# Kernel tuning notes

Hardware: AMD Instinct MI355X
Metric: run time of the kernel (lower is better)

The kernel has to match this reference:

```python
import jax, jax.numpy as jnp
import numpy as np

D, ED, N, R, K, NL = 128, 256, 16, 8, 4, 3   # d_model, d_inner, d_state, dt_rank, d_conv, n_layers
B, L = 4, 1024
HID, OUT = 256, 2
EPS = 1e-5


def setup_inputs() -> dict:
    key = jax.random.key(0)
    ks = jax.random.split(key, 16)
    g = lambda k, shape, s=0.05: jax.random.normal(k, shape, dtype=jnp.float32) * s
    return {
        "x": jax.random.normal(ks[0], (B, L, D), dtype=jnp.float32),
        # Mamba params, stacked over (2 directions, NL layers)
        "rms_w": jnp.ones((2, NL, D), jnp.float32),
        "in_w": g(ks[1], (2, NL, 2 * ED, D)),
        "in_b": g(ks[2], (2, NL, 2 * ED)),
        "conv_w": g(ks[3], (2, NL, ED, K)),
        "conv_b": g(ks[4], (2, NL, ED)),
        "xproj_w": g(ks[5], (2, NL, R + 2 * N, ED)),
        "dt_w": g(ks[6], (2, NL, ED, R)),
        "dt_b": g(ks[7], (2, NL, ED)),
        "A_log": jnp.broadcast_to(jnp.log(jnp.arange(1.0, N + 1.0, dtype=jnp.float32)), (2, NL, ED, N)) + 0.0,
        "Dp": jnp.ones((2, NL, ED), jnp.float32),
        "out_w": g(ks[8], (2, NL, D, ED)),
        "out_b": g(ks[9], (2, NL, D)),
        # MLP head params (BatchNorm in training mode: batch stats)
        "bn1_g": jnp.ones((2 * D,), jnp.float32), "bn1_b": jnp.zeros((2 * D,), jnp.float32),
        "w1": g(ks[10], (HID, 2 * D)), "b1": g(ks[11], (HID,)),
        "bn2_g": jnp.ones((HID,), jnp.float32), "bn2_b": jnp.zeros((HID,), jnp.float32),
        "w2": g(ks[12], (HID, HID)), "b2": g(ks[13], (HID,)),
        "bn3_g": jnp.ones((HID,), jnp.float32), "bn3_b": jnp.zeros((HID,), jnp.float32),
        "w3": g(ks[14], (OUT, HID)), "b3": g(ks[15], (OUT,)),
    }


def _rms(x, w):
    return x * jax.lax.rsqrt(jnp.mean(x * x, axis=-1, keepdims=True) + EPS) * w


def _dwconv(x, w, b):
    # causal depthwise conv; x: (B,L,ED), w: (ED,K)
    y = jax.lax.conv_general_dilated(x.transpose(0, 2, 1), w[:, None, :], (1,), [(K - 1, 0)],
                                     feature_group_count=ED, dimension_numbers=("NCH", "OIH", "NCH"))
    return y.transpose(0, 2, 1) + b


def _ssm(dA, dBx, C):
    # dA,dBx: (B,L,ED,N); C: (B,L,N) -> y: (B,L,ED)
    def step(h, inp):
        a, bx, c = inp
        h = a * h + bx
        return h, jnp.einsum("ben,bn->be", h, c)
    h0 = jnp.zeros((dA.shape[0], ED, N), dA.dtype)
    _, ys = jax.lax.scan(step, h0, (dA.transpose(1, 0, 2, 3), dBx.transpose(1, 0, 2, 3), C.transpose(1, 0, 2)))
    return ys.transpose(1, 0, 2)


def _block(x, in_w, in_b, conv_w, conv_b, xproj_w, dt_w, dt_b, A_log, Dp, out_w, out_b):
    xz = x @ in_w.T + in_b
    xi, z = xz[..., :ED], xz[..., ED:]
    xi = jax.nn.silu(_dwconv(xi, conv_w, conv_b))
    dbc = xi @ xproj_w.T
    dt, Bm, Cm = dbc[..., :R], dbc[..., R:R + N], dbc[..., R + N:]
    delta = jax.nn.softplus(dt @ dt_w.T + dt_b)            # (B,L,ED)
    A = -jnp.exp(A_log)                                    # (ED,N)
    dA = jnp.exp(delta[..., None] * A)                     # (B,L,ED,N)
    dBx = (delta * xi)[..., None] * Bm[:, :, None, :]      # (B,L,ED,N)
    y = _ssm(dA, dBx, Cm) + Dp * xi
    y = y * jax.nn.silu(z)
    return y @ out_w.T + out_b


def _mamba(x, d, rms_w, in_w, in_b, conv_w, conv_b, xproj_w, dt_w, dt_b, A_log, Dp, out_w, out_b):
    for l in range(NL):
        x = x + _block(_rms(x, rms_w[d, l]), in_w[d, l], in_b[d, l], conv_w[d, l], conv_b[d, l],
                       xproj_w[d, l], dt_w[d, l], dt_b[d, l], A_log[d, l], Dp[d, l], out_w[d, l], out_b[d, l])
    return x


def _bn(x, g, b):
    m = jnp.mean(x, axis=0)
    v = jnp.mean((x - m) ** 2, axis=0)  # biased var, torch BN training mode
    return (x - m) * jax.lax.rsqrt(v + EPS) * g + b


def _forward(x, rms_w, in_w, in_b, conv_w, conv_b, xproj_w, dt_w, dt_b, A_log, Dp, out_w, out_b,
             bn1_g, bn1_b, w1, b1, bn2_g, bn2_b, w2, b2, bn3_g, bn3_b, w3, b3):
    mp = (rms_w, in_w, in_b, conv_w, conv_b, xproj_w, dt_w, dt_b, A_log, Dp, out_w, out_b)
    fwd = _mamba(x, 0, *mp)
    bwd = jnp.flip(_mamba(jnp.flip(x, axis=1), 1, *mp), axis=1)
    h = jnp.concatenate([fwd, bwd], axis=2).reshape(B * L, 2 * D)
    h = jax.nn.leaky_relu(_bn(h, bn1_g, bn1_b) @ w1.T + b1)
    h = jax.nn.leaky_relu(_bn(h, bn2_g, bn2_b) @ w2.T + b2)
    h = _bn(h, bn3_g, bn3_b) @ w3.T + b3
    return h.reshape(B, L, OUT)


def reference(x, rms_w, in_w, in_b, conv_w, conv_b, xproj_w, dt_w, dt_b, A_log, Dp, out_w, out_b,
              bn1_g, bn1_b, w1, b1, bn2_g, bn2_b, w2, b2, bn3_g, bn3_b, w3, b3):
    return _forward(x, rms_w, in_w, in_b, conv_w, conv_b, xproj_w, dt_w, dt_b, A_log, Dp, out_w, out_b,
                    bn1_g, bn1_b, w1, b1, bn2_g, bn2_b, w2, b2, bn3_g, bn3_b, w3, b3)
```

## Files before the change

kernel.cpp:

```cpp
#include <hip/hip_runtime.h>
#include <hip/hip_bf16.h>
#include <hip/hip_fp16.h>

#define NL 3
#define EPS 1e-5f

#define C_INB    393984L
#define C_CONVW  397056L
#define C_CONVB  403200L
#define C_XPROJW 404736L
#define C_DTW    466176L
#define C_DTB    478464L
#define C_ALOG   480000L
#define C_DP     504576L
#define C_OUTB   702720L
#define C_BN1G   703488L
#define C_BN1B   703744L
#define C_B1     769536L
#define C_BN2G   769792L
#define C_BN2B   770048L
#define C_B2     835840L
#define C_BN3G   836096L
#define C_BN3B   836352L
#define C_W3     836608L
#define C_B3     837120L
#define FLAG_OFF 837184L
#define X0_OFF   837248L
#define X1_OFF   1361536L
#define XZT_OFF  1885824L
#define DBCT_OFF 8177280L
#define YGP_OFF  8504960L
#define BNA_OFF  10603648L
#define HINW_OFF  10605184L
#define HOUTW_OFF 10801792L
#define HW1_OFF   10900096L
#define HW2_OFF   10932864L
#define HXW_OFF   10965632L
#define H1_OFF   XZT_OFF
#define H2_OFF   (XZT_OFF + 1048576L)

#define ASLD 68

struct Ptrs { const void* p[25]; };

typedef _Float16 half8 __attribute__((ext_vector_type(8)));
typedef float f32x4 __attribute__((ext_vector_type(4)));

static __device__ const int  CV_SRC[21] = {0,0,3,4,5,6,7,8,9,10,12,13,14,16,17,18,20,21,22,23,24};
static __device__ const long CV_DST[21] = {X0_OFF,X1_OFF,C_INB,C_CONVW,C_CONVB,C_XPROJW,C_DTW,C_DTB,C_ALOG,C_DP,
                                           C_OUTB,C_BN1G,C_BN1B,C_B1,C_BN2G,C_BN2B,C_B2,C_BN3G,C_BN3B,C_W3,C_B3};
static __device__ const int  CV_SZ[21]  = {524288,524288,3072,6144,1536,61440,12288,1536,24576,1536,
                                           768,256,256,256,256,256,256,256,256,512,2};

__device__ inline float ldsrc(const void* s, long i, bool isbf) {
  if (isbf) { unsigned int u = ((const unsigned short*)s)[i]; return __uint_as_float(u << 16); }
  return ((const float*)s)[i];
}

__global__ __launch_bounds__(256) void g_convert(Ptrs ps, float* __restrict__ ws) {
  bool isbf = (*(const unsigned int*)ps.p[1]) == 0x3F803F80u;
  int job = blockIdx.y;
  if (job == 0 && blockIdx.x == 0 && threadIdx.x == 0) ws[FLAG_OFF] = isbf ? 1.f : 0.f;
  int tid0 = blockIdx.x * 256 + threadIdx.x;
  int stride = gridDim.x * 256;
  if (job < 21) {
    int n = CV_SZ[job];
    const void* s = ps.p[CV_SRC[job]];
    float* dp = ws + CV_DST[job];
    bool permute = (job < 2);
    for (int i = tid0; i < n; i += stride) {
      long si = i;
      if (permute) {
        int row = i >> 7, col = i & 127;
        int b = row >> 10, p = row & 1023;
        int t = ((p & 63) << 4) + (p >> 6);
        si = ((long)((b << 10) + t) << 7) + col;
      }
      dp[i] = ldsrc(s, si, isbf);
    }
  } else if (job == 21) {
    _Float16* dp = (_Float16*)(ws + HINW_OFF);
    const void* sw = ps.p[2]; const void* sr = ps.p[1];
    for (int i = tid0; i < 393216; i += stride) {
      int dl = i >> 16, k = i & 127;
      float v = ldsrc(sw, i, isbf) * ldsrc(sr, dl*128 + k, isbf);
      dp[i] = (_Float16)v;
    }
  } else if (job == 22) {
    _Float16* dp = (_Float16*)(ws + HOUTW_OFF);
    const void* s = ps.p[11];
    for (int i = tid0; i < 196608; i += stride) dp[i] = (_Float16)ldsrc(s, i, isbf);
  } else if (job == 23) {
    _Float16* dp = (_Float16*)(ws + HW1_OFF);
    const void* s = ps.p[15];
    for (int i = tid0; i < 65536; i += stride) dp[i] = (_Float16)ldsrc(s, i, isbf);
  } else if (job == 24) {
    _Float16* dp = (_Float16*)(ws + HW2_OFF);
    const void* s = ps.p[19];
    for (int i = tid0; i < 65536; i += stride) dp[i] = (_Float16)ldsrc(s, i, isbf);
  } else if (job == 25) {
    for (int i = tid0; i < 1536; i += stride) ws[BNA_OFF + i] = 0.f;
  } else {
    _Float16* dp = (_Float16*)(ws + HXW_OFF);
    const void* s = ps.p[5];
    for (int i = tid0; i < 98304; i += stride) {
      int dl = i >> 14;
      int rem = i & 16383;
      int nn = rem >> 8, k = rem & 255;
      float v = (nn < 40) ? ldsrc(s, (long)(dl*40+nn)*256 + k, isbf) : 0.f;
      dp[i] = (_Float16)v;
    }
  }
}

__device__ inline void mm_inner(const float* As, const float* Bs, float4* acc) {
  int tx = threadIdx.x & 15, ty = threadIdx.x >> 4;
  #pragma unroll
  for (int k = 0; k < 64; ++k) {
    float4 av = *(const float4*)&As[k*ASLD + ty*4];
    float4 bv = *(const float4*)&Bs[k*ASLD + tx*4];
    acc[0].x = fmaf(av.x,bv.x,acc[0].x); acc[0].y = fmaf(av.x,bv.y,acc[0].y); acc[0].z = fmaf(av.x,bv.z,acc[0].z); acc[0].w = fmaf(av.x,bv.w,acc[0].w);
    acc[1].x = fmaf(av.y,bv.x,acc[1].x); acc[1].y = fmaf(av.y,bv.y,acc[1].y); acc[1].z = fmaf(av.y,bv.z,acc[1].z); acc[1].w = fmaf(av.y,bv.w,acc[1].w);
    acc[2].x = fmaf(av.z,bv.x,acc[2].x); acc[2].y = fmaf(av.z,bv.y,acc[2].y); acc[2].z = fmaf(av.z,bv.z,acc[2].z); acc[2].w = fmaf(av.z,bv.w,acc[2].w);
    acc[3].x = fmaf(av.w,bv.x,acc[3].x); acc[3].y = fmaf(av.w,bv.y,acc[3].y); acc[3].z = fmaf(av.w,bv.z,acc[3].z); acc[3].w = fmaf(av.w,bv.w,acc[3].w);
  }
}

__device__ inline void stageT_g(float* S, const float* src, int ld, int row0, int k0, int nvalid) {
  int m = threadIdx.x >> 2, q = threadIdx.x & 3;
  const float* p = src + (long)(row0 + m) * ld + k0 + q*16;
  bool ok = (row0 + m) < nvalid;
  #pragma unroll
  for (int j = 0; j < 4; ++j) {
    float4 v = ok ? *(const float4*)(p + j*4) : make_float4(0.f,0.f,0.f,0.f);
    int kk = q*16 + j*4;
    S[(kk+0)*ASLD+m] = v.x; S[(kk+1)*ASLD+m] = v.y; S[(kk+2)*ASLD+m] = v.z; S[(kk+3)*ASLD+m] = v.w;
  }
}

__device__ inline float softplusf(float x) {
  if (x > 20.f) return x;
  return __logf(1.f + __expf(x));
}
__device__ inline float siluf(float a) { return a / (1.f + __expf(-a)); }

__global__ __launch_bounds__(256) void g_k1m(float* __restrict__ ws, int layer) {
  int d = blockIdx.z, nt = blockIdx.y, pt = blockIdx.x;
  const float* X = ws + (d ? X1_OFF : X0_OFF);
  const _Float16* Wf = (const _Float16*)(ws + HINW_OFF) + (long)(d*NL+layer)*65536;
  const float* Bi = ws + C_INB + (d*NL+layer)*512;
  __shared__ float rsq[256];
  __shared__ float rsc[64];
  int p0 = pt*64;
  {
    int row = threadIdx.x >> 2, q = threadIdx.x & 3;
    const float* xp = X + (long)(p0+row)*128 + q*32;
    float s = 0.f;
    #pragma unroll
    for (int j = 0; j < 8; ++j) {
      float4 v = *(const float4*)(xp + j*4);
      s += v.x*v.x + v.y*v.y + v.z*v.z + v.w*v.w;
    }
    rsq[row*4+q] = s;
  }
  __syncthreads();
  if (threadIdx.x < 64) {
    float s = rsq[threadIdx.x*4] + rsq[threadIdx.x*4+1] + rsq[threadIdx.x*4+2] + rsq[threadIdx.x*4+3];
    rsc[threadIdx.x] = rsqrtf(s * (1.f/128.f) + EPS);
  }
  __syncthreads();
  int w = threadIdx.x >> 6, lane = threadIdx.x & 63;
  int quad = lane >> 4, lm = lane & 15;
  int n0 = nt*64 + w*16;
  f32x4 zero = {0.f,0.f,0.f,0.f};
  f32x4 acc[4] = {zero, zero, zero, zero};
  #pragma unroll
  for (int s = 0; s < 4; ++s) {
    int k0 = s*32 + quad*8;
    half8 af = *(const half8*)(Wf + (long)(n0+lm)*128 + k0);
    #pragma unroll
    for (int t = 0; t < 4; ++t) {
      int pr = t*16 + lm;
      const float* xp = X + (long)(p0+pr)*128 + k0;
      float4 v0 = *(const float4*)xp;
      float4 v1 = *(const float4*)(xp+4);
      float r = rsc[pr];
      half8 bf;
      bf[0]=(_Float16)(v0.x*r); bf[1]=(_Float16)(v0.y*r); bf[2]=(_Float16)(v0.z*r); bf[3]=(_Float16)(v0.w*r);
      bf[4]=(_Float16)(v1.x*r); bf[5]=(_Float16)(v1.y*r); bf[6]=(_Float16)(v1.z*r); bf[7]=(_Float16)(v1.w*r);
      acc[t] = __builtin_amdgcn_mfma_f32_16x16x32_f16(af, bf, acc[t], 0, 0, 0);
    }
  }
  float* xzt = ws + XZT_OFF + (long)d*2097152L;
  #pragma unroll
  for (int r = 0; r < 4; ++r) {
    int n = n0 + quad*4 + r;
    float bias = Bi[n];
    #pragma unroll
    for (int t = 0; t < 4; ++t) {
      int p = p0 + t*16 + lm;
      xzt[(long)n*4096 + p] = acc[t][r] + bias;
    }
  }
}

#define AHLD 264
__global__ __launch_bounds__(256) void g_k3m(float* __restrict__ ws, int layer) {
  int d = blockIdx.z, b = blockIdx.y;
  int ii = blockIdx.x >> 1, c0 = (blockIdx.x & 1) * 32;
  const float* xz = ws + XZT_OFF + (long)d*2097152L;
  const float* cw = ws + C_CONVW + (long)(d*NL+layer)*1024;
  const float* cbp = ws + C_CONVB + (d*NL+layer)*256;
  const _Float16* Wx = (const _Float16*)(ws + HXW_OFF) + (long)(d*NL+layer)*16384;
  __shared__ __align__(16) _Float16 Ah[32*AHLD];
  int col[4], sh[4];
  col[0] = ii; sh[0] = 0;
  #pragma unroll
  for (int j = 1; j < 4; ++j) {
    if (d == 0) { if (ii-j >= 0) { col[j]=ii-j; sh[j]=0; } else { col[j]=ii-j+16; sh[j]=-1; } }
    else        { if (ii+j <= 15){ col[j]=ii+j; sh[j]=0; } else { col[j]=ii+j-16; sh[j]=1; } }
  }
  int c = threadIdx.x & 31, eh = threadIdx.x >> 5;
  int gc = c0 + c;
  long rowbase = (long)b*1024;
  for (int r = 0; r < 32; ++r) {
    int e = eh*32 + r;
    const float* xrow = xz + (long)e*4096 + rowbase;
    float4 cwv = *(const float4*)(cw + e*4);
    float v0 = xrow[col[0]*64 + gc];
    float v1, v2, v3;
    {
      bool bad = (sh[1] < 0 && gc == 0) || (sh[1] > 0 && gc == 63);
      v1 = bad ? 0.f : xrow[col[1]*64 + gc + sh[1]];
    }
    {
      bool bad = (sh[2] < 0 && gc == 0) || (sh[2] > 0 && gc == 63);
      v2 = bad ? 0.f : xrow[col[2]*64 + gc + sh[2]];
    }
    {
      bool bad = (sh[3] < 0 && gc == 0) || (sh[3] > 0 && gc == 63);
      v3 = bad ? 0.f : xrow[col[3]*64 + gc + sh[3]];
    }
    float a = cbp[e] + cwv.w*v0 + cwv.z*v1 + cwv.y*v2 + cwv.x*v3;
    Ah[c*AHLD + e] = (_Float16)siluf(a);
  }
  __syncthreads();
  int w = threadIdx.x >> 6, lane = threadIdx.x & 63;
  int quad = lane >> 4, lm = lane & 15;
  f32x4 zero = {0.f,0.f,0.f,0.f};
  f32x4 acc[2] = {zero, zero};
  #pragma unroll
  for (int s = 0; s < 8; ++s) {
    int k0 = s*32 + quad*8;
    half8 af = *(const half8*)(Wx + (long)(w*16+lm)*256 + k0);
    #pragma unroll
    for (int t = 0; t < 2; ++t) {
      half8 bf = *(const half8*)(&Ah[(t*16+lm)*AHLD + k0]);
      acc[t] = __builtin_amdgcn_mfma_f32_16x16x32_f16(af, bf, acc[t], 0, 0, 0);
    }
  }
  float* dbcT = ws + DBCT_OFF + (long)d*163840L;
  long P0 = (long)b*1024 + ii*64 + c0;
  #pragma unroll
  for (int t = 0; t < 2; ++t) {
    #pragma unroll
    for (int r = 0; r < 4; ++r) {
      int n = w*16 + quad*4 + r;
      if (n < 40) dbcT[(long)n*4096 + P0 + t*16 + lm] = acc[t][r];
    }
  }
}

__global__ __launch_bounds__(256) void g_k5c(float* __restrict__ ws, int layer) {
  int d = blockIdx.z, b = blockIdx.y, eg = blockIdx.x;
  int es = threadIdx.x >> 6;
  int c  = threadIdx.x & 63;
  int e = eg*4 + es;
  int g0 = b*1024 + c;
  const float* xzrow = ws + XZT_OFF + (long)d*2097152L + (long)e*4096 + g0;
  const float* zp    = ws + XZT_OFF + (long)d*2097152L + (long)(256+e)*4096 + g0;
  const float* dbc = ws + DBCT_OFF + (long)d*163840L + g0;
  float*       yo  = ws + YGP_OFF + (long)d*1048576L + (long)e*4096 + g0;
  const float* dw = ws + C_DTW + (long)((d*NL+layer)*256 + e)*8;
  float dtb = ws[C_DTB + (d*NL+layer)*256 + e];
  const float* al = ws + C_ALOG + (long)((d*NL+layer)*256 + e)*16;
  float Dpe = ws[C_DP + (d*NL+layer)*256 + e];
  float4 cwv = *(const float4*)(ws + C_CONVW + (long)((d*NL+layer)*256 + e)*4);
  float cb = ws[C_CONVB + (d*NL+layer)*256 + e];
  float dtw[8];
  #pragma unroll
  for (int n = 0; n < 8; ++n) dtw[n] = dw[n];
  float Anv[16]; bool fast = true;
  #pragma unroll
  for (int n = 0; n < 16; ++n) {
    Anv[n] = -__expf(al[n]);
    fast = fast && (fabsf(Anv[n] + (float)(n+1)) < 1e-3f * (float)(n+1));
  }
  float w1, w2, w3;
  if (d == 0) {
    if (c > 0) { w1 = xzrow[959]; w2 = xzrow[895]; w3 = xzrow[831]; }
    else { w1 = w2 = w3 = 0.f; }
  } else {
    if (c < 63) { w1 = xzrow[1]; w2 = xzrow[65]; w3 = xzrow[129]; }
    else { w1 = w2 = w3 = 0.f; }
  }
  __shared__ float aL[4*64*17];
  __shared__ float hL[4*64*17];
  float h[16], ap[16], del[16], xcv[16];
  float Q = 1.f;
  #pragma unroll
  for (int n = 0; n < 16; ++n) { h[n] = 0.f; ap[n] = 1.f; }
  int i0 = d ? 15 : 0, di = d ? -1 : 1;
  for (int s = 0; s < 16; ++s) {
    int i = i0 + s*di;
    int off = i*64;
    float a0 = dtb;
    #pragma unroll
    for (int n = 0; n < 8; ++n) a0 += dbc[(long)n*4096 + off] * dtw[n];
    float dl = softplusf(a0);
    float xt = xzrow[off];
    float xc = siluf(cb + cwv.w*xt + cwv.z*w1 + cwv.y*w2 + cwv.x*w3);
    w3 = w2; w2 = w1; w1 = xt;
    del[s] = dl; xcv[s] = xc;
    float dx = dl * xc;
    if (fast) {
      float q = __expf(-dl);
      float qp[16];
      qp[0]=q; qp[1]=q*q; qp[2]=qp[1]*q; qp[3]=qp[1]*qp[1];
      float q4=qp[3];
      qp[4]=qp[0]*q4; qp[5]=qp[1]*q4; qp[6]=qp[2]*q4; qp[7]=q4*q4;
      float q8=qp[7];
      #pragma unroll
      for (int j = 0; j < 8; ++j) qp[8+j]=qp[j]*q8;
      Q *= q;
      #pragma unroll
      for (int n = 0; n < 16; ++n)
        h[n] = fmaf(qp[n], h[n], dx * dbc[(long)(8+n)*4096 + off]);
    } else {
      #pragma unroll
      for (int n = 0; n < 16; ++n) {
        float a = __expf(dl * Anv[n]);
        ap[n] *= a;
        h[n] = fmaf(a, h[n], dx * dbc[(long)(8+n)*4096 + off]);
      }
    }
  }
  if (fast) {
    float p = Q;
    #pragma unroll
    for (int n = 0; n < 16; ++n) { ap[n] = p; p *= Q; }
  }
  int base = (es*64 + c)*17;
  #pragma unroll
  for (int n = 0; n < 16; ++n) { aL[base+n] = ap[n]; hL[base+n] = h[n]; }
  __syncthreads();
  if (threadIdx.x < 64) {
    int e2 = threadIdx.x >> 4, n = threadIdx.x & 15;
    float h0 = 0.f;
    for (int s2 = 0; s2 < 64; ++s2) {
      int cc = d ? (63 - s2) : s2;
      int ix = (e2*64 + cc)*17 + n;
      float ta = aL[ix], th = hL[ix];
      aL[ix] = h0;
      h0 = fmaf(ta, h0, th);
    }
  }
  __syncthreads();
  #pragma unroll
  for (int n = 0; n < 16; ++n) h[n] = aL[base+n];
  for (int s = 0; s < 16; ++s) {
    int i = i0 + s*di;
    int off = i*64;
    float dl = del[s], xc = xcv[s];
    float dx = dl * xc;
    float zr = zp[off];
    float zg = zr / (1.f + __expf(-zr));
    float ya[4] = {0.f,0.f,0.f,0.f};
    if (fast) {
      float q = __expf(-dl);
      float qp[16];
      qp[0]=q; qp[1]=q*q; qp[2]=qp[1]*q; qp[3]=qp[1]*qp[1];
      float q4=qp[3];
      qp[4]=qp[0]*q4; qp[5]=qp[1]*q4; qp[6]=qp[2]*q4; qp[7]=q4*q4;
      float q8=qp[7];
      #pragma unroll
      for (int j = 0; j < 8; ++j) qp[8+j]=qp[j]*q8;
      #pragma unroll
      for (int n = 0; n < 16; ++n) {
        h[n] = fmaf(qp[n], h[n], dx * dbc[(long)(8+n)*4096 + off]);
        ya[n & 3] = fmaf(h[n], dbc[(long)(24+n)*4096 + off], ya[n & 3]);
      }
    } else {
      #pragma unroll
      for (int n = 0; n < 16; ++n) {
        float a = __expf(dl * Anv[n]);
        h[n] = fmaf(a, h[n], dx * dbc[(long)(8+n)*4096 + off]);
        ya[n & 3] = fmaf(h[n], dbc[(long)(24+n)*4096 + off], ya[n & 3]);
      }
    }
    float y = (ya[0] + ya[1]) + (ya[2] + ya[3]);
    y = fmaf(Dpe, xc, y);
    yo[off] = y * zg;
  }
}

__global__ __launch_bounds__(256) void g_k61(float* __restrict__ ws, int layer) {
  int d = blockIdx.z, pt = blockIdx.x;
  int p0 = pt*16;
  const float* Y = ws + YGP_OFF + (long)d*1048576L;
  const _Float16* Wf = (const _Float16*)(ws + HOUTW_OFF) + (long)(d*NL+layer)*32768;
  const float* Ob = ws + C_OUTB + (d*NL+layer)*128;
  float* Xd = ws + (d ? X1_OFF : X0_OFF);
  __shared__ __align__(16) _Float16 Ah[16*264];
  __shared__ float Xn[16*137];
  __shared__ float rsq[64];
  __shared__ float rsc[16];
  {
    int e = threadIdx.x;
    const float* yp = Y + (long)e*4096 + p0;
    float4 v0 = *(const float4*)yp;
    float4 v1 = *(const float4*)(yp+4);
    float4 v2 = *(const float4*)(yp+8);
    float4 v3 = *(const float4*)(yp+12);
    float vv[16] = {v0.x,v0.y,v0.z,v0.w, v1.x,v1.y,v1.z,v1.w,
                    v2.x,v2.y,v2.z,v2.w, v3.x,v3.y,v3.z,v3.w};
    #pragma unroll
    for (int p = 0; p < 16; ++p) Ah[p*264 + e] = (_Float16)vv[p];
  }
  __syncthreads();
  int w = threadIdx.x >> 6, lane = threadIdx.x & 63;
  int quad = lane >> 4, lm = lane & 15;
  f32x4 zero = {0.f,0.f,0.f,0.f};
  f32x4 acc[2] = {zero, zero};
  #pragma unroll
  for (int s = 0; s < 8; ++s) {
    int k0 = s*32 + quad*8;
    half8 af = *(const half8*)(&Ah[lm*264 + k0]);
    #pragma unroll
    for (int t = 0; t < 2; ++t) {
      int n = w*32 + t*16 + lm;
      half8 bf = *(const half8*)(Wf + (long)n*256 + k0);
      acc[t] = __builtin_amdgcn_mfma_f32_16x16x32_f16(af, bf, acc[t], 0, 0, 0);
    }
  }
  bool dostats = (layer == NL-1);
  float* bna = ws + BNA_OFF;
  #pragma unroll
  for (int t = 0; t < 2; ++t) {
    int n = w*32 + t*16 + lm;
    float ob = Ob[n];
    float s1 = 0.f, s2 = 0.f;
    #pragma unroll
    for (int r = 0; r < 4; ++r) {
      int p = p0 + quad*4 + r;
      float v = acc[t][r] + ob + Xd[(long)p*128 + n];
      Xd[(long)p*128 + n] = v;
      Xn[(quad*4 + r)*137 + n] = v;
      s1 += v; s2 += v*v;
    }
    if (dostats) {
      s1 += __shfl_xor(s1, 16, 64); s2 += __shfl_xor(s2, 16, 64);
      s1 += __shfl_xor(s1, 32, 64); s2 += __shfl_xor(s2, 32, 64);
      if (quad == 0) {
        int ch = d*128 + n;
        atomicAdd(&bna[ch], s1);
        atomicAdd(&bna[256 + ch], s2);
      }
    }
  }
  if (layer == NL-1) return;
  __syncthreads();
  if (threadIdx.x < 64) {
    int pl = threadIdx.x >> 2, qq = threadIdx.x & 3;
    float s = 0.f;
    const float* xr = &Xn[pl*137 + qq*32];
    #pragma unroll
    for (int k = 0; k < 32; ++k) s += xr[k]*xr[k];
    rsq[threadIdx.x] = s;
  }
  __syncthreads();
  if (threadIdx.x < 16) {
    float s = rsq[threadIdx.x*4] + rsq[threadIdx.x*4+1] + rsq[threadIdx.x*4+2] + rsq[threadIdx.x*4+3];
    rsc[threadIdx.x] = rsqrtf(s * (1.f/128.f) + EPS);
  }
  __syncthreads();
  const _Float16* Wn = (const _Float16*)(ws + HINW_OFF) + (long)(d*NL+layer+1)*65536;
  const float* Bi = ws + C_INB + (d*NL+layer+1)*512;
  f32x4 acc2[8] = {zero,zero,zero,zero,zero,zero,zero,zero};
  float r = rsc[lm];
  #pragma unroll
  for (int s = 0; s < 4; ++s) {
    int k0 = s*32 + quad*8;
    half8 bf;
    const float* xr = &Xn[lm*137 + k0];
    #pragma unroll
    for (int j = 0; j < 8; ++j) bf[j] = (_Float16)(xr[j] * r);
    #pragma unroll
    for (int tt = 0; tt < 8; ++tt) {
      int n2 = w*128 + tt*16 + lm;
      half8 af = *(const half8*)(Wn + (long)n2*128 + k0);
      acc2[tt] = __builtin_amdgcn_mfma_f32_16x16x32_f16(af, bf, acc2[tt], 0, 0, 0);
    }
  }
  float* xzt = ws + XZT_OFF + (long)d*2097152L;
  #pragma unroll
  for (int tt = 0; tt < 8; ++tt) {
    #pragma unroll
    for (int rr = 0; rr < 4; ++rr) {
      int n2 = w*128 + tt*16 + quad*4 + rr;
      xzt[(long)n2*4096 + p0 + lm] = acc2[tt][rr] + Bi[n2];
    }
  }
}

template<int STAGE>
__global__ __launch_bounds__(256) void g_hgm(float* __restrict__ ws) {
  int p0 = blockIdx.x * 16;
  __shared__ float scL[256], shL[256];
  {
    int k = threadIdx.x;
    float S = ws[BNA_OFF + STAGE*512 + k], S2 = ws[BNA_OFF + STAGE*512 + 256 + k];
    float mean = S * (1.f/4096.f);
    float var = S2 * (1.f/4096.f) - mean*mean;
    const float* g = ws + (STAGE == 0 ? C_BN1G : C_BN2G);
    const float* bb = ws + (STAGE == 0 ? C_BN1B : C_BN2B);
    float sc = g[k] * rsqrtf(var + EPS);
    scL[k] = sc; shL[k] = bb[k] - mean*sc;
  }
  __syncthreads();
  const _Float16* Wf = (const _Float16*)(ws + (STAGE == 0 ? HW1_OFF : HW2_OFF));
  const float* bias = ws + (STAGE == 0 ? C_B1 : C_B2);
  float* H = ws + (STAGE == 0 ? H1_OFF : H2_OFF);
  int w = threadIdx.x >> 6, lane = threadIdx.x & 63;
  int quad = lane >> 4, lm = lane & 15;
  f32x4 zero = {0.f,0.f,0.f,0.f};
  f32x4 acc[4] = {zero, zero, zero, zero};
  #pragma unroll
  for (int s = 0; s < 8; ++s) {
    int k0 = s*32 + quad*8;
    const float* src;
    if (STAGE == 0) src = (k0 < 128) ? (ws + X0_OFF + (long)(p0+lm)*128 + k0)
                                     : (ws + X1_OFF + (long)(p0+lm)*128 + (k0-128));
    else            src = ws + H1_OFF + (long)(p0+lm)*256 + k0;
    float4 v0 = *(const float4*)src, v1 = *(const float4*)(src+4);
    float4 c0 = *(const float4*)&scL[k0], c1 = *(const float4*)&scL[k0+4];
    float4 h0 = *(const float4*)&shL[k0], h1 = *(const float4*)&shL[k0+4];
    half8 af;
    af[0]=(_Float16)(v0.x*c0.x+h0.x); af[1]=(_Float16)(v0.y*c0.y+h0.y);
    af[2]=(_Float16)(v0.z*c0.z+h0.z); af[3]=(_Float16)(v0.w*c0.w+h0.w);
    af[4]=(_Float16)(v1.x*c1.x+h1.x); af[5]=(_Float16)(v1.y*c1.y+h1.y);
    af[6]=(_Float16)(v1.z*c1.z+h1.z); af[7]=(_Float16)(v1.w*c1.w+h1.w);
    #pragma unroll
    for (int t = 0; t < 4; ++t) {
      int n = w*64 + t*16 + lm;
      half8 bf = *(const half8*)(Wf + (long)n*256 + k0);
      acc[t] = __builtin_amdgcn_mfma_f32_16x16x32_f16(af, bf, acc[t], 0, 0, 0);
    }
  }
  float* bna = ws + BNA_OFF + (STAGE+1)*512;
  #pragma unroll
  for (int t = 0; t < 4; ++t) {
    int n = w*64 + t*16 + lm;
    float bs = bias[n];
    float s1 = 0.f, s2 = 0.f;
    #pragma unroll
    for (int r = 0; r < 4; ++r) {
      int p = p0 + quad*4 + r;
      float v = acc[t][r] + bs;
      v = v > 0.f ? v : 0.01f*v;
      H[(long)p*256 + n] = v;
      s1 += v; s2 += v*v;
    }
    s1 += __shfl_xor(s1, 16, 64); s2 += __shfl_xor(s2, 16, 64);
    s1 += __shfl_xor(s1, 32, 64); s2 += __shfl_xor(s2, 32, 64);
    if (quad == 0) {
      atomicAdd(&bna[n], s1);
      atomicAdd(&bna[256 + n], s2);
    }
  }
}

__global__ __launch_bounds__(256) void g_hg2(float* __restrict__ ws, void* dout) {
  int mt = blockIdx.x;
  __shared__ float As[64*ASLD];
  __shared__ float Bs[64*ASLD];
  __shared__ float scL[256], shL[256];
  {
    int k = threadIdx.x;
    float S = ws[BNA_OFF + 2*512 + k], S2 = ws[BNA_OFF + 2*512 + 256 + k];
    float mean = S * (1.f/4096.f);
    float var = S2 * (1.f/4096.f) - mean*mean;
    float sc = ws[C_BN3G + k] * rsqrtf(var + EPS);
    scL[k] = sc; shL[k] = ws[C_BN3B + k] - mean*sc;
  }
  __syncthreads();
  float4 acc[4] = {make_float4(0,0,0,0),make_float4(0,0,0,0),make_float4(0,0,0,0),make_float4(0,0,0,0)};
  for (int kt = 0; kt < 4; ++kt) {
    int k0 = kt * 64;
    {
      int m = threadIdx.x >> 2, q = threadIdx.x & 3;
      const float* p = ws + H2_OFF + (long)(mt*64 + m)*256 + k0 + q*16;
      #pragma unroll
      for (int j = 0; j < 4; ++j) {
        float4 v  = *(const float4*)(p + j*4);
        float4 s4 = *(const float4*)&scL[k0 + q*16 + j*4];
        float4 h4 = *(const float4*)&shL[k0 + q*16 + j*4];
        int kk = q*16 + j*4;
        As[(kk+0)*ASLD+m] = v.x*s4.x + h4.x; As[(kk+1)*ASLD+m] = v.y*s4.y + h4.y;
        As[(kk+2)*ASLD+m] = v.z*s4.z + h4.z; As[(kk+3)*ASLD+m] = v.w*s4.w + h4.w;
      }
    }
    stageT_g(Bs, ws + C_W3, 256, 0, k0, 2);
    __syncthreads();
    mm_inner(As, Bs, acc);
    __syncthreads();
  }
  int tx = threadIdx.x & 15, ty = threadIdx.x >> 4;
  if (tx == 0) {
    bool isbf = ws[FLAG_OFF] != 0.f;
    float b0 = ws[C_B3], b1 = ws[C_B3 + 1];
    #pragma unroll
    for (int i = 0; i < 4; ++i) {
      int r = mt*64 + ty*4 + i;
      int b = r >> 10, p = r & 1023;
      int t = ((p & 63) << 4) + (p >> 6);
      long tok = (long)(b << 10) + t;
      float v0 = acc[i].x + b0, v1 = acc[i].y + b1;
      if (isbf) {
        __hip_bfloat16* o = (__hip_bfloat16*)dout;
        o[tok*2]   = __float2bfloat16(v0);
        o[tok*2+1] = __float2bfloat16(v1);
      } else {
        float* o = (float*)dout;
        o[tok*2] = v0; o[tok*2+1] = v1;
      }
    }
  }
}

extern "C" void kernel_launch(void* const* d_in, const int* in_sizes, int n_in,
                              void* d_out, int out_size, void* d_ws, size_t ws_size,
                              hipStream_t stream) {
  (void)in_sizes; (void)n_in; (void)out_size; (void)ws_size;
  float* ws = (float*)d_ws;
  Ptrs ps;
  for (int i = 0; i < 25; ++i) ps.p[i] = d_in[i];
  g_convert<<<dim3(32, 27), dim3(256), 0, stream>>>(ps, ws);
  g_k1m<<<dim3(64, 8, 2), dim3(256), 0, stream>>>(ws, 0);
  for (int l = 0; l < NL; ++l) {
    g_k3m<<<dim3(32, 4, 2), dim3(256), 0, stream>>>(ws, l);
    g_k5c<<<dim3(64, 4, 2), dim3(256), 0, stream>>>(ws, l);
    g_k61<<<dim3(256, 1, 2), dim3(256), 0, stream>>>(ws, l);
  }
  g_hgm<0><<<dim3(256), dim3(256), 0, stream>>>(ws);
  g_hgm<1><<<dim3(256), dim3(256), 0, stream>>>(ws);
  g_hg2<<<dim3(64), dim3(256), 0, stream>>>(ws, d_out);
}
```

Before: 405.2 us.

## Fuse input conversion into in-projection, retile conv kernel, drop specialized scan path

The separate conversion kernel and the first in-projection kernel are merged into one launch. The in-projection now reads the raw x, rms and weight inputs directly, applies the sequence permutation on the fly, and writes the permuted x as a side effect. The depthwise-conv plus x_proj kernel is retiled to 16 columns per block with twice as many blocks, and the x_proj weight source index is changed from input 5 to input 6. The scan's fast path, which replaced per-state exponentials with powers of one exponential when A matched -(n+1), is removed, so every step now computes 16 exponentials again.

```diff
diff --git a/kernel.cpp b/kernel.cpp
--- a/kernel.cpp
+++ b/kernel.cpp
@@ -8,7 +8,6 @@
 #define C_INB    393984L
 #define C_CONVW  397056L
 #define C_CONVB  403200L
-#define C_XPROJW 404736L
 #define C_DTW    466176L
 #define C_DTB    478464L
 #define C_ALOG   480000L
@@ -46,96 +45,25 @@
 typedef _Float16 half8 __attribute__((ext_vector_type(8)));
 typedef float f32x4 __attribute__((ext_vector_type(4)));
 
-static __device__ const int  CV_SRC[21] = {0,0,3,4,5,6,7,8,9,10,12,13,14,16,17,18,20,21,22,23,24};
-static __device__ const long CV_DST[21] = {X0_OFF,X1_OFF,C_INB,C_CONVW,C_CONVB,C_XPROJW,C_DTW,C_DTB,C_ALOG,C_DP,
-                                           C_OUTB,C_BN1G,C_BN1B,C_B1,C_BN2G,C_BN2B,C_B2,C_BN3G,C_BN3B,C_W3,C_B3};
-static __device__ const int  CV_SZ[21]  = {524288,524288,3072,6144,1536,61440,12288,1536,24576,1536,
-                                           768,256,256,256,256,256,256,256,256,512,2};
+static __device__ const int  CJ_SRC[18] = {3,4,5,7,8,9,10,12,13,14,16,17,18,20,21,22,23,24};
+static __device__ const long CJ_DST[18] = {C_INB,C_CONVW,C_CONVB,C_DTW,C_DTB,C_ALOG,C_DP,C_OUTB,
+                                           C_BN1G,C_BN1B,C_B1,C_BN2G,C_BN2B,C_B2,C_BN3G,C_BN3B,C_W3,C_B3};
+static __device__ const int  CJ_SZ[18]  = {3072,6144,1536,12288,1536,24576,1536,768,
+                                           256,256,256,256,256,256,256,256,512,2};
 
 __device__ inline float ldsrc(const void* s, long i, bool isbf) {
   if (isbf) { unsigned int u = ((const unsigned short*)s)[i]; return __uint_as_float(u << 16); }
   return ((const float*)s)[i];
 }
 
-__global__ __launch_bounds__(256) void g_convert(Ptrs ps, float* __restrict__ ws) {
-  bool isbf = (*(const unsigned int*)ps.p[1]) == 0x3F803F80u;
-  int job = blockIdx.y;
-  if (job == 0 && blockIdx.x == 0 && threadIdx.x == 0) ws[FLAG_OFF] = isbf ? 1.f : 0.f;
-  int tid0 = blockIdx.x * 256 + threadIdx.x;
-  int stride = gridDim.x * 256;
-  if (job < 21) {
-    int n = CV_SZ[job];
-    const void* s = ps.p[CV_SRC[job]];
-    float* dp = ws + CV_DST[job];
-    bool permute = (job < 2);
-    for (int i = tid0; i < n; i += stride) {
-      long si = i;
-      if (permute) {
-        int row = i >> 7, col = i & 127;
-        int b = row >> 10, p = row & 1023;
-        int t = ((p & 63) << 4) + (p >> 6);
-        si = ((long)((b << 10) + t) << 7) + col;
-      }
-      dp[i] = ldsrc(s, si, isbf);
-    }
-  } else if (job == 21) {
-    _Float16* dp = (_Float16*)(ws + HINW_OFF);
-    const void* sw = ps.p[2]; const void* sr = ps.p[1];
-    for (int i = tid0; i < 393216; i += stride) {
-      int dl = i >> 16, k = i & 127;
-      float v = ldsrc(sw, i, isbf) * ldsrc(sr, dl*128 + k, isbf);
-      dp[i] = (_Float16)v;
-    }
-  } else if (job == 22) {
-    _Float16* dp = (_Float16*)(ws + HOUTW_OFF);
-    const void* s = ps.p[11];
-    for (int i = tid0; i < 196608; i += stride) dp[i] = (_Float16)ldsrc(s, i, isbf);
-  } else if (job == 23) {
-    _Float16* dp = (_Float16*)(ws + HW1_OFF);
-    const void* s = ps.p[15];
-    for (int i = tid0; i < 65536; i += stride) dp[i] = (_Float16)ldsrc(s, i, isbf);
-  } else if (job == 24) {
-    _Float16* dp = (_Float16*)(ws + HW2_OFF);
-    const void* s = ps.p[19];
-    for (int i = tid0; i < 65536; i += stride) dp[i] = (_Float16)ldsrc(s, i, isbf);
-  } else if (job == 25) {
-    for (int i = tid0; i < 1536; i += stride) ws[BNA_OFF + i] = 0.f;
-  } else {
-    _Float16* dp = (_Float16*)(ws + HXW_OFF);
-    const void* s = ps.p[5];
-    for (int i = tid0; i < 98304; i += stride) {
-      int dl = i >> 14;
-      int rem = i & 16383;
-      int nn = rem >> 8, k = rem & 255;
-      float v = (nn < 40) ? ldsrc(s, (long)(dl*40+nn)*256 + k, isbf) : 0.f;
-      dp[i] = (_Float16)v;
-    }
-  }
-}
-
-__device__ inline void mm_inner(const float* As, const float* Bs, float4* acc) {
-  int tx = threadIdx.x & 15, ty = threadIdx.x >> 4;
-  #pragma unroll
-  for (int k = 0; k < 64; ++k) {
-    float4 av = *(const float4*)&As[k*ASLD + ty*4];
-    float4 bv = *(const float4*)&Bs[k*ASLD + tx*4];
-    acc[0].x = fmaf(av.x,bv.x,acc[0].x); acc[0].y = fmaf(av.x,bv.y,acc[0].y); acc[0].z = fmaf(av.x,bv.z,acc[0].z); acc[0].w = fmaf(av.x,bv.w,acc[0].w);
-    acc[1].x = fmaf(av.y,bv.x,acc[1].x); acc[1].y = fmaf(av.y,bv.y,acc[1].y); acc[1].z = fmaf(av.y,bv.z,acc[1].z); acc[1].w = fmaf(av.y,bv.w,acc[1].w);
-    acc[2].x = fmaf(av.z,bv.x,acc[2].x); acc[2].y = fmaf(av.z,bv.y,acc[2].y); acc[2].z = fmaf(av.z,bv.z,acc[2].z); acc[2].w = fmaf(av.z,bv.w,acc[2].w);
-    acc[3].x = fmaf(av.w,bv.x,acc[3].x); acc[3].y = fmaf(av.w,bv.y,acc[3].y); acc[3].z = fmaf(av.w,bv.z,acc[3].z); acc[3].w = fmaf(av.w,bv.w,acc[3].w);
-  }
-}
-
-__device__ inline void stageT_g(float* S, const float* src, int ld, int row0, int k0, int nvalid) {
-  int m = threadIdx.x >> 2, q = threadIdx.x & 3;
-  const float* p = src + (long)(row0 + m) * ld + k0 + q*16;
-  bool ok = (row0 + m) < nvalid;
-  #pragma unroll
-  for (int j = 0; j < 4; ++j) {
-    float4 v = ok ? *(const float4*)(p + j*4) : make_float4(0.f,0.f,0.f,0.f);
-    int kk = q*16 + j*4;
-    S[(kk+0)*ASLD+m] = v.x; S[(kk+1)*ASLD+m] = v.y; S[(kk+2)*ASLD+m] = v.z; S[(kk+3)*ASLD+m] = v.w;
-  }
+__device__ inline float4 ld4(const void* s, long i, bool isbf) {
+  if (isbf) {
+    const unsigned short* u = (const unsigned short*)s + i;
+    ushort4 uv = *(const ushort4*)u;
+    return make_float4(__uint_as_float((unsigned)uv.x << 16), __uint_as_float((unsigned)uv.y << 16),
+                       __uint_as_float((unsigned)uv.z << 16), __uint_as_float((unsigned)uv.w << 16));
+  }
+  return *(const float4*)((const float*)s + i);
 }
 
 __device__ inline float softplusf(float x) {
@@ -144,22 +72,75 @@
 }
 __device__ inline float siluf(float a) { return a / (1.f + __expf(-a)); }
 
-__global__ __launch_bounds__(256) void g_k1m(float* __restrict__ ws, int layer) {
-  int d = blockIdx.z, nt = blockIdx.y, pt = blockIdx.x;
-  const float* X = ws + (d ? X1_OFF : X0_OFF);
-  const _Float16* Wf = (const _Float16*)(ws + HINW_OFF) + (long)(d*NL+layer)*65536;
-  const float* Bi = ws + C_INB + (d*NL+layer)*512;
+__global__ __launch_bounds__(256) void g_cvk1(Ptrs ps, float* __restrict__ ws) {
+  bool isbf = (*(const unsigned int*)ps.p[1]) == 0x3F803F80u;
+  int blk = blockIdx.x;
+  if (blk >= 1024) {
+    int jb = blk - 1024;
+    int job = jb >> 3;
+    int tid0 = (jb & 7) * 256 + threadIdx.x;
+    int stride = 2048;
+    if (jb == 0 && threadIdx.x == 0) ws[FLAG_OFF] = isbf ? 1.f : 0.f;
+    if (job < 18) {
+      int n = CJ_SZ[job];
+      const void* s = ps.p[CJ_SRC[job]];
+      float* dp = ws + CJ_DST[job];
+      for (int i = tid0; i < n; i += stride) dp[i] = ldsrc(s, i, isbf);
+    } else if (job == 18) {
+      _Float16* dp = (_Float16*)(ws + HINW_OFF);
+      const void* sw = ps.p[2]; const void* sr = ps.p[1];
+      for (int i = tid0; i < 393216; i += stride) {
+        int dl = i >> 16, k = i & 127;
+        dp[i] = (_Float16)(ldsrc(sw, i, isbf) * ldsrc(sr, dl*128 + k, isbf));
+      }
+    } else if (job == 19) {
+      _Float16* dp = (_Float16*)(ws + HOUTW_OFF);
+      const void* s = ps.p[11];
+      for (int i = tid0; i < 196608; i += stride) dp[i] = (_Float16)ldsrc(s, i, isbf);
+    } else if (job == 20) {
+      _Float16* dp = (_Float16*)(ws + HW1_OFF);
+      const void* s = ps.p[15];
+      for (int i = tid0; i < 65536; i += stride) dp[i] = (_Float16)ldsrc(s, i, isbf);
+    } else if (job == 21) {
+      _Float16* dp = (_Float16*)(ws + HW2_OFF);
+      const void* s = ps.p[19];
+      for (int i = tid0; i < 65536; i += stride) dp[i] = (_Float16)ldsrc(s, i, isbf);
+    } else if (job == 22) {
+      _Float16* dp = (_Float16*)(ws + HXW_OFF);
+      const void* s = ps.p[6];
+      for (int i = tid0; i < 98304; i += stride) {
+        int dl = i >> 14;
+        int rem = i & 16383;
+        int nn = rem >> 8, k = rem & 255;
+        float v = (nn < 40) ? ldsrc(s, (long)(dl*40+nn)*256 + k, isbf) : 0.f;
+        dp[i] = (_Float16)v;
+      }
+    } else {
+      for (int i = tid0; i < 1536; i += stride) ws[BNA_OFF + i] = 0.f;
+    }
+    return;
+  }
+  int pt = blk & 63, nt = (blk >> 6) & 7, d = blk >> 9;
+  const void* xraw = ps.p[0];
+  const void* wraw = ps.p[2];
+  const void* rraw = ps.p[1];
+  const float* Bi = ws + C_INB + (d*NL)*512;
+  float* Xout = ws + (d ? X1_OFF : X0_OFF);
   __shared__ float rsq[256];
   __shared__ float rsc[64];
   int p0 = pt*64;
   {
     int row = threadIdx.x >> 2, q = threadIdx.x & 3;
-    const float* xp = X + (long)(p0+row)*128 + q*32;
+    int pb = p0 + row;
+    int bb = pb >> 10, pl = pb & 1023;
+    int t = ((pl & 63) << 4) + (pl >> 6);
+    long si = ((long)((bb << 10) + t)) * 128 + q*32;
     float s = 0.f;
     #pragma unroll
     for (int j = 0; j < 8; ++j) {
-      float4 v = *(const float4*)(xp + j*4);
+      float4 v = ld4(xraw, si + j*4, isbf);
       s += v.x*v.x + v.y*v.y + v.z*v.z + v.w*v.w;
+      if (nt == 0) *(float4*)&Xout[(long)pb*128 + q*32 + j*4] = v;
     }
     rsq[row*4+q] = s;
   }
@@ -174,17 +155,34 @@
   int n0 = nt*64 + w*16;
   f32x4 zero = {0.f,0.f,0.f,0.f};
   f32x4 acc[4] = {zero, zero, zero, zero};
+  long sib[4]; float rr[4];
+  #pragma unroll
+  for (int t = 0; t < 4; ++t) {
+    int pb = p0 + t*16 + lm;
+    int bb = pb >> 10, pl = pb & 1023;
+    int tt = ((pl & 63) << 4) + (pl >> 6);
+    sib[t] = ((long)((bb << 10) + tt)) * 128;
+    rr[t] = rsc[t*16 + lm];
+  }
+  long wbase = ((long)((d*NL)*512) + n0 + lm) * 128;
+  long rbase = (long)(d*NL)*128;
   #pragma unroll
   for (int s = 0; s < 4; ++s) {
     int k0 = s*32 + quad*8;
-    half8 af = *(const half8*)(Wf + (long)(n0+lm)*128 + k0);
+    float4 w0 = ld4(wraw, wbase + k0, isbf);
+    float4 w1 = ld4(wraw, wbase + k0 + 4, isbf);
+    float4 r0 = ld4(rraw, rbase + k0, isbf);
+    float4 r1 = ld4(rraw, rbase + k0 + 4, isbf);
+    half8 af;
+    af[0]=(_Float16)(w0.x*r0.x); af[1]=(_Float16)(w0.y*r0.y);
+    af[2]=(_Float16)(w0.z*r0.z); af[3]=(_Float16)(w0.w*r0.w);
+    af[4]=(_Float16)(w1.x*r1.x); af[5]=(_Float16)(w1.y*r1.y);
+    af[6]=(_Float16)(w1.z*r1.z); af[7]=(_Float16)(w1.w*r1.w);
     #pragma unroll
     for (int t = 0; t < 4; ++t) {
-      int pr = t*16 + lm;
-      const float* xp = X + (long)(p0+pr)*128 + k0;
-      float4 v0 = *(const float4*)xp;
-      float4 v1 = *(const float4*)(xp+4);
-      float r = rsc[pr];
+      float4 v0 = ld4(xraw, sib[t] + k0, isbf);
+      float4 v1 = ld4(xraw, sib[t] + k0 + 4, isbf);
+      float r = rr[t];
       half8 bf;
       bf[0]=(_Float16)(v0.x*r); bf[1]=(_Float16)(v0.y*r); bf[2]=(_Float16)(v0.z*r); bf[3]=(_Float16)(v0.w*r);
       bf[4]=(_Float16)(v1.x*r); bf[5]=(_Float16)(v1.y*r); bf[6]=(_Float16)(v1.z*r); bf[7]=(_Float16)(v1.w*r);
@@ -199,7 +197,7 @@
     #pragma unroll
     for (int t = 0; t < 4; ++t) {
       int p = p0 + t*16 + lm;
-      xzt[(long)n*4096 + p] = acc[t][r] + bias;
+      xzt[(long)n*4096 + p] = acc[r == r ? t : t][r] + bias;
     }
   }
 }
@@ -207,12 +205,12 @@
 #define AHLD 264
 __global__ __launch_bounds__(256) void g_k3m(float* __restrict__ ws, int layer) {
   int d = blockIdx.z, b = blockIdx.y;
-  int ii = blockIdx.x >> 1, c0 = (blockIdx.x & 1) * 32;
+  int ii = blockIdx.x >> 2, c0 = (blockIdx.x & 3) * 16;
   const float* xz = ws + XZT_OFF + (long)d*2097152L;
   const float* cw = ws + C_CONVW + (long)(d*NL+layer)*1024;
   const float* cbp = ws + C_CONVB + (d*NL+layer)*256;
   const _Float16* Wx = (const _Float16*)(ws + HXW_OFF) + (long)(d*NL+layer)*16384;
-  __shared__ __align__(16) _Float16 Ah[32*AHLD];
+  __shared__ __align__(16) _Float16 Ah[16*AHLD];
   int col[4], sh[4];
   col[0] = ii; sh[0] = 0;
   #pragma unroll
@@ -220,54 +218,41 @@
     if (d == 0) { if (ii-j >= 0) { col[j]=ii-j; sh[j]=0; } else { col[j]=ii-j+16; sh[j]=-1; } }
     else        { if (ii+j <= 15){ col[j]=ii+j; sh[j]=0; } else { col[j]=ii+j-16; sh[j]=1; } }
   }
-  int c = threadIdx.x & 31, eh = threadIdx.x >> 5;
+  int c = threadIdx.x & 15, eh = threadIdx.x >> 4;
   int gc = c0 + c;
   long rowbase = (long)b*1024;
-  for (int r = 0; r < 32; ++r) {
-    int e = eh*32 + r;
+  #pragma unroll 4
+  for (int r = 0; r < 16; ++r) {
+    int e = eh*16 + r;
     const float* xrow = xz + (long)e*4096 + rowbase;
     float4 cwv = *(const float4*)(cw + e*4);
     float v0 = xrow[col[0]*64 + gc];
-    float v1, v2, v3;
-    {
-      bool bad = (sh[1] < 0 && gc == 0) || (sh[1] > 0 && gc == 63);
-      v1 = bad ? 0.f : xrow[col[1]*64 + gc + sh[1]];
-    }
-    {
-      bool bad = (sh[2] < 0 && gc == 0) || (sh[2] > 0 && gc == 63);
-      v2 = bad ? 0.f : xrow[col[2]*64 + gc + sh[2]];
-    }
-    {
-      bool bad = (sh[3] < 0 && gc == 0) || (sh[3] > 0 && gc == 63);
-      v3 = bad ? 0.f : xrow[col[3]*64 + gc + sh[3]];
-    }
+    bool b1 = (sh[1] < 0 && gc == 0) || (sh[1] > 0 && gc == 63);
+    bool b2 = (sh[2] < 0 && gc == 0) || (sh[2] > 0 && gc == 63);
+    bool b3 = (sh[3] < 0 && gc == 0) || (sh[3] > 0 && gc == 63);
+    float v1 = b1 ? 0.f : xrow[col[1]*64 + gc + sh[1]];
+    float v2 = b2 ? 0.f : xrow[col[2]*64 + gc + sh[2]];
+    float v3 = b3 ? 0.f : xrow[col[3]*64 + gc + sh[3]];
     float a = cbp[e] + cwv.w*v0 + cwv.z*v1 + cwv.y*v2 + cwv.x*v3;
     Ah[c*AHLD + e] = (_Float16)siluf(a);
   }
   __syncthreads();
   int w = threadIdx.x >> 6, lane = threadIdx.x & 63;
   int quad = lane >> 4, lm = lane & 15;
-  f32x4 zero = {0.f,0.f,0.f,0.f};
-  f32x4 acc[2] = {zero, zero};
+  f32x4 acc = {0.f,0.f,0.f,0.f};
   #pragma unroll
   for (int s = 0; s < 8; ++s) {
     int k0 = s*32 + quad*8;
     half8 af = *(const half8*)(Wx + (long)(w*16+lm)*256 + k0);
-    #pragma unroll
-    for (int t = 0; t < 2; ++t) {
-      half8 bf = *(const half8*)(&Ah[(t*16+lm)*AHLD + k0]);
-      acc[t] = __builtin_amdgcn_mfma_f32_16x16x32_f16(af, bf, acc[t], 0, 0, 0);
-    }
+    half8 bf = *(const half8*)(&Ah[lm*AHLD + k0]);
+    acc = __builtin_amdgcn_mfma_f32_16x16x32_f16(af, bf, acc, 0, 0, 0);
   }
   float* dbcT = ws + DBCT_OFF + (long)d*163840L;
   long P0 = (long)b*1024 + ii*64 + c0;
   #pragma unroll
-  for (int t = 0; t < 2; ++t) {
-    #pragma unroll
-    for (int r = 0; r < 4; ++r) {
-      int n = w*16 + quad*4 + r;
-      if (n < 40) dbcT[(long)n*4096 + P0 + t*16 + lm] = acc[t][r];
-    }
+  for (int r = 0; r < 4; ++r) {
+    int n = w*16 + quad*4 + r;
+    if (n < 40) dbcT[(long)n*4096 + P0 + lm] = acc[r];
   }
 }
 
@@ -290,12 +275,9 @@
   float dtw[8];
   #pragma unroll
   for (int n = 0; n < 8; ++n) dtw[n] = dw[n];
-  float Anv[16]; bool fast = true;
-  #pragma unroll
-  for (int n = 0; n < 16; ++n) {
-    Anv[n] = -__expf(al[n]);
-    fast = fast && (fabsf(Anv[n] + (float)(n+1)) < 1e-3f * (float)(n+1));
-  }
+  float Anv[16];
+  #pragma unroll
+  for (int n = 0; n < 16; ++n) Anv[n] = -__expf(al[n]);
   float w1, w2, w3;
   if (d == 0) {
     if (c > 0) { w1 = xzrow[959]; w2 = xzrow[895]; w3 = xzrow[831]; }
@@ -307,7 +289,6 @@
   __shared__ float aL[4*64*17];
   __shared__ float hL[4*64*17];
   float h[16], ap[16], del[16], xcv[16];
-  float Q = 1.f;
   #pragma unroll
   for (int n = 0; n < 16; ++n) { h[n] = 0.f; ap[n] = 1.f; }
   int i0 = d ? 15 : 0, di = d ? -1 : 1;
@@ -323,32 +304,12 @@
     w3 = w2; w2 = w1; w1 = xt;
     del[s] = dl; xcv[s] = xc;
     float dx = dl * xc;
-    if (fast) {
-      float q = __expf(-dl);
-      float qp[16];
-      qp[0]=q; qp[1]=q*q; qp[2]=qp[1]*q; qp[3]=qp[1]*qp[1];
-      float q4=qp[3];
-      qp[4]=qp[0]*q4; qp[5]=qp[1]*q4; qp[6]=qp[2]*q4; qp[7]=q4*q4;
-      float q8=qp[7];
-      #pragma unroll
-      for (int j = 0; j < 8; ++j) qp[8+j]=qp[j]*q8;
-      Q *= q;
-      #pragma unroll
-      for (int n = 0; n < 16; ++n)
-        h[n] = fmaf(qp[n], h[n], dx * dbc[(long)(8+n)*4096 + off]);
-    } else {
-      #pragma unroll
-      for (int n = 0; n < 16; ++n) {
-        float a = __expf(dl * Anv[n]);
-        ap[n] *= a;
-        h[n] = fmaf(a, h[n], dx * dbc[(long)(8+n)*4096 + off]);
-      }
-    }
-  }
-  if (fast) {
-    float p = Q;
-    #pragma unroll
-    for (int n = 0; n < 16; ++n) { ap[n] = p; p *= Q; }
+    #pragma unroll
+    for (int n = 0; n < 16; ++n) {
+      float a = __expf(dl * Anv[n]);
+      ap[n] *= a;
+      h[n] = fmaf(a, h[n], dx * dbc[(long)(8+n)*4096 + off]);
+    }
   }
   int base = (es*64 + c)*17;
   #pragma unroll
@@ -376,27 +337,11 @@
     float zr = zp[off];
     float zg = zr / (1.f + __expf(-zr));
     float ya[4] = {0.f,0.f,0.f,0.f};
-    if (fast) {
-      float q = __expf(-dl);
-      float qp[16];
-      qp[0]=q; qp[1]=q*q; qp[2]=qp[1]*q; qp[3]=qp[1]*qp[1];
-      float q4=qp[3];
-      qp[4]=qp[0]*q4; qp[5]=qp[1]*q4; qp[6]=qp[2]*q4; qp[7]=q4*q4;
-      float q8=qp[7];
-      #pragma unroll
-      for (int j = 0; j < 8; ++j) qp[8+j]=qp[j]*q8;
-      #pragma unroll
-      for (int n = 0; n < 16; ++n) {
-        h[n] = fmaf(qp[n], h[n], dx * dbc[(long)(8+n)*4096 + off]);
-        ya[n & 3] = fmaf(h[n], dbc[(long)(24+n)*4096 + off], ya[n & 3]);
-      }
-    } else {
-      #pragma unroll
-      for (int n = 0; n < 16; ++n) {
-        float a = __expf(dl * Anv[n]);
-        h[n] = fmaf(a, h[n], dx * dbc[(long)(8+n)*4096 + off]);
-        ya[n & 3] = fmaf(h[n], dbc[(long)(24+n)*4096 + off], ya[n & 3]);
-      }
+    #pragma unroll
+    for (int n = 0; n < 16; ++n) {
+      float a = __expf(dl * Anv[n]);
+      h[n] = fmaf(a, h[n], dx * dbc[(long)(8+n)*4096 + off]);
+      ya[n & 3] = fmaf(h[n], dbc[(long)(24+n)*4096 + off], ya[n & 3]);
     }
     float y = (ya[0] + ya[1]) + (ya[2] + ya[3]);
     y = fmaf(Dpe, xc, y);
@@ -580,6 +525,31 @@
   }
 }
 
+__device__ inline void mm_inner(const float* As, const float* Bs, float4* acc) {
+  int tx = threadIdx.x & 15, ty = threadIdx.x >> 4;
+  #pragma unroll
+  for (int k = 0; k < 64; ++k) {
+    float4 av = *(const float4*)&As[k*ASLD + ty*4];
+    float4 bv = *(const float4*)&Bs[k*ASLD + tx*4];
+    acc[0].x = fmaf(av.x,bv.x,acc[0].x); acc[0].y = fmaf(av.x,bv.y,acc[0].y); acc[0].z = fmaf(av.x,bv.z,acc[0].z); acc[0].w = fmaf(av.x,bv.w,acc[0].w);
+    acc[1].x = fmaf(av.y,bv.x,acc[1].x); acc[1].y = fmaf(av.y,bv.y,acc[1].y); acc[1].z = fmaf(av.y,bv.z,acc[1].z); acc[1].w = fmaf(av.y,bv.w,acc[1].w);
+    acc[2].x = fmaf(av.z,bv.x,acc[2].x); acc[2].y = fmaf(av.z,bv.y,acc[2].y); acc[2].z = fmaf(av.z,bv.z,acc[2].z); acc[2].w = fmaf(av.z,bv.w,acc[2].w);
+    acc[3].x = fmaf(av.w,bv.x,acc[3].x); acc[3].y = fmaf(av.w,bv.y,acc[3].y); acc[3].z = fmaf(av.w,bv.z,acc[3].z); acc[3].w = fmaf(av.w,bv.w,acc[3].w);
+  }
+}
+
+__device__ inline void stageT_g(float* S, const float* src, int ld, int row0, int k0, int nvalid) {
+  int m = threadIdx.x >> 2, q = threadIdx.x & 3;
+  const float* p = src + (long)(row0 + m) * ld + k0 + q*16;
+  bool ok = (row0 + m) < nvalid;
+  #pragma unroll
+  for (int j = 0; j < 4; ++j) {
+    float4 v = ok ? *(const float4*)(p + j*4) : make_float4(0.f,0.f,0.f,0.f);
+    int kk = q*16 + j*4;
+    S[(kk+0)*ASLD+m] = v.x; S[(kk+1)*ASLD+m] = v.y; S[(kk+2)*ASLD+m] = v.z; S[(kk+3)*ASLD+m] = v.w;
+  }
+}
+
 __global__ __launch_bounds__(256) void g_hg2(float* __restrict__ ws, void* dout) {
   int mt = blockIdx.x;
   __shared__ float As[64*ASLD];
@@ -645,10 +615,9 @@
   float* ws = (float*)d_ws;
   Ptrs ps;
   for (int i = 0; i < 25; ++i) ps.p[i] = d_in[i];
-  g_convert<<<dim3(32, 27), dim3(256), 0, stream>>>(ps, ws);
-  g_k1m<<<dim3(64, 8, 2), dim3(256), 0, stream>>>(ws, 0);
+  g_cvk1<<<dim3(1216), dim3(256), 0, stream>>>(ps, ws);
   for (int l = 0; l < NL; ++l) {
-    g_k3m<<<dim3(32, 4, 2), dim3(256), 0, stream>>>(ws, l);
+    g_k3m<<<dim3(64, 4, 2), dim3(256), 0, stream>>>(ws, l);
     g_k5c<<<dim3(64, 4, 2), dim3(256), 0, stream>>>(ws, l);
     g_k61<<<dim3(256, 1, 2), dim3(256), 0, stream>>>(ws, l);
   }
```

Result: slower. 565.5 us (+39.5%).
